# Optimization experiments

Hardware: AMD Instinct MI355X
Metric: run time of the kernel (lower is better)

## Reference

```python
import jax, jax.numpy as jnp
import numpy as np

B, S, E, H, M = 4, 2048, 1024, 16, 32  # batch, seq, hidden, heads, max_rel_dist
D = E // H  # head dim


def setup_inputs() -> dict:
    key = jax.random.key(0)
    ks = jax.random.split(key, 4)
    x = jax.random.normal(ks[0], (B, S, E), dtype=jnp.float32)
    in_proj_w = jax.random.normal(ks[1], (3 * E, E), dtype=jnp.float32) * (E ** -0.5)
    in_proj_b = jnp.zeros((3 * E,), dtype=jnp.float32)
    out_w = jax.random.normal(ks[2], (E, E), dtype=jnp.float32) * (E ** -0.5)
    out_b = jnp.zeros((E,), dtype=jnp.float32)
    rel_bias = jax.random.normal(ks[3], (2 * M + 1, H), dtype=jnp.float32) * 0.02
    return {"x": x, "in_proj_w": in_proj_w, "in_proj_b": in_proj_b,
            "out_w": out_w, "out_b": out_b, "rel_bias": rel_bias}


def reference(x, in_proj_w, in_proj_b, out_w, out_b, rel_bias):
    b, s, e = x.shape
    # relative position index: clamp(i-j, -M, M) + M  -> [S, S]
    rel_pos = jnp.clip(jnp.arange(s)[:, None] - jnp.arange(s)[None, :], -M, M) + M
    # gather per-head bias then average over heads (matches the per-head sum / H loop)
    attn_mask = rel_bias[rel_pos].mean(axis=-1)  # [S, S]

    # fused QKV projection (torch in_proj: x @ W^T + b)
    qkv = x @ in_proj_w.T + in_proj_b  # [B, S, 3E]
    q, k, v = jnp.split(qkv, 3, axis=-1)
    # reshape to heads: [B, H, S, D]
    q = q.reshape(b, s, H, D).transpose(0, 2, 1, 3)
    k = k.reshape(b, s, H, D).transpose(0, 2, 1, 3)
    v = v.reshape(b, s, H, D).transpose(0, 2, 1, 3)

    scores = jnp.einsum("bhqd,bhkd->bhqk", q, k) * (D ** -0.5) + attn_mask
    attn = jax.nn.softmax(scores, axis=-1)
    out = jnp.einsum("bhqk,bhkd->bhqd", attn, v)  # [B, H, S, D]
    out = out.transpose(0, 2, 1, 3).reshape(b, s, e)
    return out @ out_w.T + out_b
```

## Files before the change

kernel.cpp:

```cpp
#include <hip/hip_runtime.h>
#include <hip/hip_fp16.h>
#include <stdint.h>
#include <stddef.h>


typedef _Float16 half8 __attribute__((ext_vector_type(8)));
typedef _Float16 half2v __attribute__((ext_vector_type(2)));
typedef float f32x4 __attribute__((ext_vector_type(4)));
typedef float f32x16 __attribute__((ext_vector_type(16)));
typedef uint32_t u32x4 __attribute__((ext_vector_type(4)));

#define MFMA16(a, b, c) __builtin_amdgcn_mfma_f32_16x16x32_f16(a, b, c, 0, 0, 0)
#define MFMA32(a, b, c) __builtin_amdgcn_mfma_f32_32x32x16_f16(a, b, c, 0, 0, 0)

__device__ static inline void gload_lds16(const void* g, void* l) {
  __builtin_amdgcn_global_load_lds(
      (const __attribute__((address_space(1))) void*)g,
      (__attribute__((address_space(3))) void*)l, 16, 0, 0);
}

__device__ static inline uint32_t pkrtz(float a, float b) {
  return __builtin_bit_cast(uint32_t, __builtin_amdgcn_cvt_pkrtz(a, b));
}

__global__ void cvt_all(const float* __restrict__ x, const float* __restrict__ w,
                        const float* __restrict__ ow, const float* __restrict__ rb,
                        __half* __restrict__ xh, __half* __restrict__ wh,
                        __half* __restrict__ owh, float* __restrict__ mbg,
                        int nx, int nw, int no) {
  if (blockIdx.x == 0 && threadIdx.x < 65) {
    float s = 0.f;
    #pragma unroll
    for (int hh = 0; hh < 16; ++hh) s += rb[threadIdx.x * 16 + hh];
    mbg[threadIdx.x] = s * (1.44269504f / 16.f);
  }
  const int total = nx + nw + no;
  int i = blockIdx.x * blockDim.x + threadIdx.x;
  const int stride = gridDim.x * blockDim.x;
  for (; i < total; i += stride) {
    const float* src; __half* dst; int j;
    if (i < nx)            { src = x;  dst = xh;  j = i; }
    else if (i < nx + nw)  { src = w;  dst = wh;  j = i - nx; }
    else                   { src = ow; dst = owh; j = i - nx - nw; }
    const float4* p = (const float4*)src + (size_t)j * 2;
    float4 a = p[0], b = p[1];
    half8 hv;
    hv[0] = (_Float16)a.x; hv[1] = (_Float16)a.y; hv[2] = (_Float16)a.z; hv[3] = (_Float16)a.w;
    hv[4] = (_Float16)b.x; hv[5] = (_Float16)b.y; hv[6] = (_Float16)b.z; hv[7] = (_Float16)b.w;
    *(half8*)(dst + (size_t)j * 8) = hv;
  }
}

template <bool OUT_HALF>
__global__ __launch_bounds__(256)
void gemm_bt(const __half* __restrict__ A, const __half* __restrict__ Bm,
             const float* __restrict__ bias, void* __restrict__ Cout,
             int Ndim, int K) {
  __shared__ __align__(16) __half As[3][128 * 32];
  __shared__ __align__(16) __half Bs[3][128 * 32];
  const int tid = threadIdx.x;
  const int lane = tid & 63;
  const int wave = tid >> 6;
  const int wr = wave >> 1, wc = wave & 1;
  const int flat = blockIdx.y * gridDim.x + blockIdx.x;
  const int cpx = (gridDim.x * gridDim.y) >> 3;
  const int nid = (flat & 7) * cpx + (flat >> 3);
  const int bn = nid % gridDim.x;
  const int bm = nid / gridDim.x;
  const int l15 = lane & 15;
  const int kseg = lane >> 4;

  const int off0 = tid * 16;
  const int mloc0 = off0 >> 6, kb0 = off0 & 63;
  const int off1 = 4096 + tid * 16;
  const int mloc1 = off1 >> 6, kb1 = off1 & 63;
  const __half* a0 = A + (size_t)(bm * 128 + mloc0) * K + (kb0 >> 1);
  const __half* a1 = A + (size_t)(bm * 128 + mloc1) * K + (kb1 >> 1);
  const __half* b0 = Bm + (size_t)(bn * 128 + mloc0) * K + (kb0 >> 1);
  const __half* b1 = Bm + (size_t)(bn * 128 + mloc1) * K + (kb1 >> 1);

  auto stage = [&](int kt, int buf) {
    char* ad = (char*)As[buf] + wave * 1024;
    char* bd = (char*)Bs[buf] + wave * 1024;
    gload_lds16(a0 + kt * 32, ad);
    gload_lds16(a1 + kt * 32, ad + 4096);
    gload_lds16(b0 + kt * 32, bd);
    gload_lds16(b1 + kt * 32, bd + 4096);
  };

  f32x4 acc[4][4];
  #pragma unroll
  for (int i = 0; i < 4; ++i)
    #pragma unroll
    for (int j = 0; j < 4; ++j) {
      acc[i][j][0] = 0.f; acc[i][j][1] = 0.f; acc[i][j][2] = 0.f; acc[i][j][3] = 0.f;
    }

  const int nk = K >> 5;
  stage(0, 0);
  stage(1, 1);

  int buf = 0;
  for (int kt = 0; kt < nk; ++kt) {
    __syncthreads();
    if (kt + 2 < nk) {
      int nb = buf + 2; if (nb >= 3) nb -= 3;
      stage(kt + 2, nb);
    }
    const __half* as = As[buf];
    const __half* bs = Bs[buf];
    half8 af[4], bf[4];
    #pragma unroll
    for (int i = 0; i < 4; ++i) {
      af[i] = *(const half8*)&as[(wr * 64 + i * 16 + l15) * 32 + kseg * 8];
      bf[i] = *(const half8*)&bs[(wc * 64 + i * 16 + l15) * 32 + kseg * 8];
    }
    #pragma unroll
    for (int i = 0; i < 4; ++i)
      #pragma unroll
      for (int j = 0; j < 4; ++j)
        acc[i][j] = MFMA16(af[i], bf[j], acc[i][j]);
    if (++buf == 3) buf = 0;
  }

  const int crow0 = bm * 128 + wr * 64;
  const int ccol0 = bn * 128 + wc * 64;
  #pragma unroll
  for (int j = 0; j < 4; ++j) {
    const int c = ccol0 + j * 16 + l15;
    const float bv = bias[c];
    #pragma unroll
    for (int i = 0; i < 4; ++i) {
      #pragma unroll
      for (int r = 0; r < 4; ++r) {
        const int row = crow0 + i * 16 + kseg * 4 + r;
        const float v = acc[i][j][r] + bv;
        if (OUT_HALF)
          ((__half*)Cout)[(size_t)row * Ndim + c] = __float2half_rn(v);
        else
          ((float*)Cout)[(size_t)row * Ndim + c] = v;
      }
    }
  }
}

#define CHUNK(sv, c) do {                                                   \
    const int base2_ = qw - kb - 16 * (c);                                  \
    float ex_[8];                                                           \
    if (base2_ >= 47) {                                                     \
      _Pragma("unroll")                                                     \
      for (int j_ = 0; j_ < 8; ++j_)                                        \
        ex_[j_] = __builtin_amdgcn_exp2f(                                   \
            fmaf(sv[8 * ((c) & 1) + j_], kscale, mbs_hi));                  \
    } else if (base2_ <= -63) {                                             \
      _Pragma("unroll")                                                     \
      for (int j_ = 0; j_ < 8; ++j_)                                        \
        ex_[j_] = __builtin_amdgcn_exp2f(                                   \
            fmaf(sv[8 * ((c) & 1) + j_], kscale, mbs_lo));                  \
    } else {                                                                \
      _Pragma("unroll")                                                     \
      for (int j_ = 0; j_ < 8; ++j_) {                                      \
        int d_ = qs - (kb + 16 * (c) + 8 * (j_ >> 2) + (j_ & 3) + 4 * hi);  \
        d_ = min(max(d_, -32), 32);                                         \
        ex_[j_] = __builtin_amdgcn_exp2f(                                   \
            fmaf(sv[8 * ((c) & 1) + j_], kscale, mb[d_ + 32]));             \
      }                                                                     \
    }                                                                       \
    _Pragma("unroll")                                                       \
    for (int j_ = 0; j_ < 8; ++j_) lp4[j_ & 3] += ex_[j_];                  \
    uint32_t QA0_ = pkrtz(ex_[0], ex_[1]);                                  \
    uint32_t QA1_ = pkrtz(ex_[2], ex_[3]);                                  \
    uint32_t QB0_ = pkrtz(ex_[4], ex_[5]);                                  \
    uint32_t QB1_ = pkrtz(ex_[6], ex_[7]);                                  \
    auto r0_ = __builtin_amdgcn_permlane32_swap(QA0_, QB0_, false, false);  \
    auto r1_ = __builtin_amdgcn_permlane32_swap(QA1_, QB1_, false, false);  \
    u32x4 uv_;                                                              \
    uv_[0] = r0_[0]; uv_[1] = r1_[0]; uv_[2] = r0_[1]; uv_[3] = r1_[1];     \
    half8 ap_ = __builtin_bit_cast(half8, uv_);                             \
    const int cby_ = (32 * (c) + 16 * hi) ^ swzv;                           \
    half8 bv0_ = *(const half8*)(vtb + l31 * 128 + cby_);                   \
    half8 bv1_ = *(const half8*)(vtb + (32 + l31) * 128 + cby_);            \
    o0 = MFMA32(ap_, bv0_, o0);                                             \
    o1 = MFMA32(ap_, bv1_, o1);                                             \
  } while (0)

__global__ __launch_bounds__(512)
void attn_kernel(const __half* __restrict__ qkv, const float* __restrict__ mb,
                 __half* __restrict__ attn_out) {
  __shared__ __align__(16) __half Ks[4][64 * 64];
  __shared__ __align__(16) __half Vts[4][64 * 64];

  const int tid = threadIdx.x;
  const int lane = tid & 63;
  const int w = tid >> 6;
  const int l31 = lane & 31;
  const int hi = lane >> 5;
  const int flat = (blockIdx.y << 3) | blockIdx.x;
  const int nid = (flat & 7) * 64 + (flat >> 3);
  const int bh = nid >> 3;
  const int b = bh >> 4, h = bh & 15;
  const int qw = (nid & 7) * 256 + w * 32;
  const int qs = qw + l31;
  const float kscale = 0.125f * 1.44269504f;
  const int swzv = (l31 & 7) << 4;

  const float mbs_lo = mb[0];
  const float mbs_hi = mb[64];

  const size_t qrow = (size_t)(b * 2048 + qs) * 3072;
  half8 bq[4];
  #pragma unroll
  for (int s = 0; s < 4; ++s)
    bq[s] = *(const half8*)&qkv[qrow + h * 64 + s * 16 + hi * 8];

  const int krow0 = tid >> 3;
  const int kcolsw = ((tid & 7) * 16) ^ ((krow0 & 7) << 4);
  const __half* kp0 = qkv + (size_t)(b * 2048 + krow0) * 3072 + 1024 + h * 64 + (kcolsw >> 1);

  const int vds = w * 8;
  const __half* vp = qkv + (size_t)(b * 2048 + lane) * 3072 + 2048 + h * 64 + vds;

  const size_t kvstep = (size_t)64 * 3072;

  f32x4 lp4 = {0.f, 0.f, 0.f, 0.f};
  f32x16 o0, o1;
  #pragma unroll
  for (int i = 0; i < 16; ++i) { o0[i] = 0.f; o1[i] = 0.f; }

  gload_lds16(kp0, (char*)Ks[0] + w * 1024);
  gload_lds16(kp0 + kvstep, (char*)Ks[1] + w * 1024);
  half8 va = *(const half8*)vp;
  half8 vb = *(const half8*)(vp + kvstep);
  #pragma unroll
  for (int e = 0; e < 8; ++e) {
    *(__half*)((char*)Vts[0] + (vds + e) * 128 + ((lane * 2) ^ (e << 4))) = (__half)va[e];
    *(__half*)((char*)Vts[1] + (vds + e) * 128 + ((lane * 2) ^ (e << 4))) = (__half)vb[e];
  }
  va = *(const half8*)(vp + 2 * kvstep);
  vb = *(const half8*)(vp + 3 * kvstep);

  auto compute_tile = [&](int kb, const char* ksb, const char* vtb) {
    f32x16 s0, s1;
    #pragma unroll
    for (int i = 0; i < 16; ++i) { s0[i] = 0.f; s1[i] = 0.f; }
    __builtin_amdgcn_s_setprio(1);
    #pragma unroll
    for (int s = 0; s < 4; ++s) {
      const int cby = (s * 32 + hi * 16) ^ swzv;
      half8 ak0 = *(const half8*)(ksb + l31 * 128 + cby);
      half8 ak1 = *(const half8*)(ksb + (32 + l31) * 128 + cby);
      s0 = MFMA32(ak0, bq[s], s0);
      s1 = MFMA32(ak1, bq[s], s1);
    }
    __builtin_amdgcn_s_setprio(0);
    __builtin_amdgcn_s_setprio(1);
    CHUNK(s0, 0);
    CHUNK(s0, 1);
    CHUNK(s1, 2);
    CHUNK(s1, 3);
    __builtin_amdgcn_s_setprio(0);
  };

  for (int kt = 0; kt < 32; kt += 2) {
    __syncthreads();

    if (kt < 30) {
      const size_t adv2 = (size_t)(kt + 2) * kvstep;
      const size_t adv3 = (size_t)(kt + 3) * kvstep;
      gload_lds16(kp0 + adv2, (char*)Ks[(kt + 2) & 3] + w * 1024);
      gload_lds16(kp0 + adv3, (char*)Ks[(kt + 3) & 3] + w * 1024);
      char* v2 = (char*)Vts[(kt + 2) & 3];
      char* v3 = (char*)Vts[(kt + 3) & 3];
      #pragma unroll
      for (int e = 0; e < 8; ++e) {
        const int sw = (lane * 2) ^ (e << 4);
        *(__half*)(v2 + (vds + e) * 128 + sw) = (__half)va[e];
        *(__half*)(v3 + (vds + e) * 128 + sw) = (__half)vb[e];
      }
      if (kt < 28) {
        va = *(const half8*)(vp + (size_t)(kt + 4) * kvstep);
        vb = *(const half8*)(vp + (size_t)(kt + 5) * kvstep);
      }
    }

    compute_tile(kt * 64, (const char*)Ks[kt & 3], (const char*)Vts[kt & 3]);
    compute_tile((kt + 1) * 64, (const char*)Ks[(kt + 1) & 3],
                 (const char*)Vts[(kt + 1) & 3]);
  }

  float lp = (lp4[0] + lp4[1]) + (lp4[2] + lp4[3]);
  lp += __shfl_xor(lp, 32, 64);
  float* lsh = ((float*)Ks[1]) + w * 32;
  if (hi == 0) lsh[l31] = lp;
  #pragma unroll
  for (int r = 0; r < 16; ++r) {
    const int ql = (r & 3) + 8 * (r >> 2) + 4 * hi;
    const float rl = 1.f / lsh[ql];
    const size_t row = (size_t)(b * 2048 + qw + ql) * 1024 + h * 64;
    attn_out[row + l31]      = __float2half(o0[r] * rl);
    attn_out[row + 32 + l31] = __float2half(o1[r] * rl);
  }
}

extern "C" void kernel_launch(void* const* d_in, const int* in_sizes, int n_in,
                              void* d_out, int out_size, void* d_ws, size_t ws_size,
                              hipStream_t stream) {
  const float* x    = (const float*)d_in[0];
  const float* in_w = (const float*)d_in[1];
  const float* in_b = (const float*)d_in[2];
  const float* ow   = (const float*)d_in[3];
  const float* ob   = (const float*)d_in[4];
  const float* rb   = (const float*)d_in[5];

  char* ws = (char*)d_ws;
  __half* xh   = (__half*)(ws);
  __half* wh   = (__half*)(ws + 16777216);
  __half* owh  = (__half*)(ws + 23068672);
  float*  mb   = (float*)(ws + 25165824);
  __half* qkvh = (__half*)(ws + 25166336);
  __half* atth = (__half*)(ws + 75497984);

  cvt_all<<<2048, 256, 0, stream>>>(x, in_w, ow, rb, xh, wh, owh, mb,
                                    (8192 * 1024) / 8, (3072 * 1024) / 8,
                                    (1024 * 1024) / 8);

  gemm_bt<true><<<dim3(24, 64), 256, 0, stream>>>(xh, wh, in_b, qkvh, 3072, 1024);
  attn_kernel<<<dim3(8, 64), 512, 0, stream>>>(qkvh, mb, atth);
  gemm_bt<false><<<dim3(8, 64), 256, 0, stream>>>(atth, owh, ob, (float*)d_out, 1024, 1024);
}
```

Baseline: 208.2 us.

## Use 256x256 tile GEMM with 512 threads for QKV projection

Adds a new fp16 MFMA GEMM kernel with 256x256 output tiles, 8 waves each computing 128x64, double-buffered LDS staging via global_load_lds, and an XCD-aware block remap. The QKV projection now uses it in place of the 128x128 tile kernel. Larger tiles raise arithmetic intensity and cut global/L2 traffic per FLOP. In exchange the kernel uses 128 KB of LDS per block, which limits occupancy, and the launch shrinks to 384 blocks, which may leave CUs underused and can cause wave quantization.

```diff
diff --git a/kernel.cpp b/kernel.cpp
--- a/kernel.cpp
+++ b/kernel.cpp
@@ -139,6 +139,105 @@
           ((__half*)Cout)[(size_t)row * Ndim + c] = __float2half_rn(v);
         else
           ((float*)Cout)[(size_t)row * Ndim + c] = v;
+      }
+    }
+  }
+}
+
+__global__ __launch_bounds__(512)
+void gemm256(const __half* __restrict__ A, const __half* __restrict__ Bm,
+             const float* __restrict__ bias, __half* __restrict__ Cout,
+             int Ndim, int K) {
+  __shared__ __align__(16) __half As[2][256 * 64];
+  __shared__ __align__(16) __half Bs[2][256 * 64];
+
+  const int tid = threadIdx.x;
+  const int lane = tid & 63;
+  const int w = tid >> 6;
+  const int wr = w >> 2, wc = w & 3;
+  const int l15 = lane & 15;
+  const int kseg = lane >> 4;
+  const int swzr = (l15 & 7) << 4;
+
+  const int flat = blockIdx.y * gridDim.x + blockIdx.x;
+  const int cpx = (gridDim.x * gridDim.y) >> 3;
+  const int nid = (flat & 7) * cpx + (flat >> 3);
+  const int bn = nid % gridDim.x;
+  const int bm = nid / gridDim.x;
+
+  const int r0 = tid >> 3;
+  const int swcolh = ((((tid & 7) * 16) ^ ((r0 & 7) << 4)) >> 1);
+  const __half* pa0 = A + (size_t)(bm * 256 + 0 * 64 + r0) * K + swcolh;
+  const __half* pa1 = A + (size_t)(bm * 256 + 1 * 64 + r0) * K + swcolh;
+  const __half* pa2 = A + (size_t)(bm * 256 + 2 * 64 + r0) * K + swcolh;
+  const __half* pa3 = A + (size_t)(bm * 256 + 3 * 64 + r0) * K + swcolh;
+  const __half* pb0 = Bm + (size_t)(bn * 256 + 0 * 64 + r0) * K + swcolh;
+  const __half* pb1 = Bm + (size_t)(bn * 256 + 1 * 64 + r0) * K + swcolh;
+  const __half* pb2 = Bm + (size_t)(bn * 256 + 2 * 64 + r0) * K + swcolh;
+  const __half* pb3 = Bm + (size_t)(bn * 256 + 3 * 64 + r0) * K + swcolh;
+
+  auto stage = [&](int kt, int buf) {
+    const int ko = kt * 64;
+    char* ad = (char*)As[buf] + w * 1024;
+    char* bd = (char*)Bs[buf] + w * 1024;
+    gload_lds16(pa0 + ko, ad);
+    gload_lds16(pa1 + ko, ad + 8192);
+    gload_lds16(pa2 + ko, ad + 16384);
+    gload_lds16(pa3 + ko, ad + 24576);
+    gload_lds16(pb0 + ko, bd);
+    gload_lds16(pb1 + ko, bd + 8192);
+    gload_lds16(pb2 + ko, bd + 16384);
+    gload_lds16(pb3 + ko, bd + 24576);
+  };
+
+  f32x4 acc[8][4];
+  #pragma unroll
+  for (int i = 0; i < 8; ++i)
+    #pragma unroll
+    for (int j = 0; j < 4; ++j) {
+      acc[i][j][0] = 0.f; acc[i][j][1] = 0.f; acc[i][j][2] = 0.f; acc[i][j][3] = 0.f;
+    }
+
+  const int nk = K >> 6;
+  stage(0, 0);
+
+  int buf = 0;
+  for (int kt = 0; kt < nk; ++kt) {
+    __syncthreads();
+    if (kt + 1 < nk) stage(kt + 1, buf ^ 1);
+    const char* as = (const char*)As[buf];
+    const char* bs = (const char*)Bs[buf];
+    #pragma unroll
+    for (int kk = 0; kk < 2; ++kk) {
+      const int cb = (kk * 64 + kseg * 16) ^ swzr;
+      half8 af[8], bf[4];
+      #pragma unroll
+      for (int i = 0; i < 8; ++i)
+        af[i] = *(const half8*)(as + (wr * 128 + i * 16 + l15) * 128 + cb);
+      #pragma unroll
+      for (int j = 0; j < 4; ++j)
+        bf[j] = *(const half8*)(bs + (wc * 64 + j * 16 + l15) * 128 + cb);
+      #pragma unroll
+      for (int i = 0; i < 8; ++i)
+        #pragma unroll
+        for (int j = 0; j < 4; ++j)
+          acc[i][j] = MFMA16(af[i], bf[j], acc[i][j]);
+    }
+    buf ^= 1;
+  }
+
+  const int crow0 = bm * 256 + wr * 128;
+  const int ccol0 = bn * 256 + wc * 64;
+  #pragma unroll
+  for (int j = 0; j < 4; ++j) {
+    const int c = ccol0 + j * 16 + l15;
+    const float bv = bias[c];
+    #pragma unroll
+    for (int i = 0; i < 8; ++i) {
+      #pragma unroll
+      for (int r = 0; r < 4; ++r) {
+        const int row = crow0 + i * 16 + kseg * 4 + r;
+        Cout[(size_t)row * Ndim + c] = __float2half_rn(acc[i][j][r] + bv);
       }
     }
   }
@@ -324,7 +423,7 @@
                                     (8192 * 1024) / 8, (3072 * 1024) / 8,
                                     (1024 * 1024) / 8);
 
-  gemm_bt<true><<<dim3(24, 64), 256, 0, stream>>>(xh, wh, in_b, qkvh, 3072, 1024);
+  gemm256<<<dim3(12, 32), 512, 0, stream>>>(xh, wh, in_b, qkvh, 3072, 1024);
   attn_kernel<<<dim3(8, 64), 512, 0, stream>>>(qkvh, mb, atth);
   gemm_bt<false><<<dim3(8, 64), 256, 0, stream>>>(atth, owh, ob, (float*)d_out, 1024, 1024);
 }
```

Measured after the change: 216.1 us. +3.8%, slower.
